# Kernel tuning notes

Measured on AMD Instinct MI355X. Metric: run time of the kernel, lower is better.

Reference implementation:

```python
import jax, jax.numpy as jnp
import numpy as np
from jax import lax

_DN = ('NCHW', 'OIHW', 'NCHW')


def _depthwise_kernel(C):
    base = jnp.array([[0.1, 0.1, 0.1], [0.1, 0.2, 0.1], [0.1, 0.1, 0.1]], jnp.float32)
    return jnp.broadcast_to(base[None, None], (C, 1, 3, 3))


def setup_inputs() -> dict:
    key = jax.random.key(0)
    k0, k1, k2 = jax.random.split(key, 3)
    T, B, C, H, W = 16, 16, 8, 128, 128
    hidden = max(1, C // 16)  # reduction_ratio = 16
    events = jax.random.normal(k0, (T, B, C, H, W), jnp.float32)
    conv_w = _depthwise_kernel(C)  # fixed neighbor kernel from _initialize_weights
    att_w1 = jax.random.normal(k1, (hidden, 2 * C), jnp.float32) / np.sqrt(2 * C)
    att_w2 = jax.random.normal(k2, (C, hidden), jnp.float32) / np.sqrt(hidden)
    return {
        'events': events,
        'conv_w': conv_w,
        'att_w1': att_w1,
        'att_w2': att_w2,
        'density_w': jnp.array(1.0, jnp.float32),
        'temporal_w': jnp.array(0.8, jnp.float32),
        'motion_w': jnp.array(0.5, jnp.float32),
    }


def _forward(events, conv_w, att_w1, att_w2, density_w, temporal_w, motion_w):
    T, B, C, H, W = events.shape
    x = events.reshape(T * B, C, H, W)
    # depthwise 3x3 neighbor conv (groups=C), batched over all T steps at once
    wi = lax.conv_general_dilated(x, conv_w, (1, 1), 'SAME',
                                  dimension_numbers=_DN, feature_group_count=C)
    # --- BALIFBetaAdaptor: max/avg pool -> 1x1 convs (== matmuls) -> sigmoid ---
    mx = jnp.max(x, axis=(2, 3))            # (TB, C)
    av = jnp.mean(x, axis=(2, 3))           # (TB, C)
    pooled = jnp.concatenate([mx, av], axis=1)  # (TB, 2C)
    h = jax.nn.relu(pooled @ att_w1.T)
    beta = (0.5 + 0.45 * jax.nn.sigmoid(h @ att_w2.T)).reshape(T, B, C, 1, 1)
    # --- LightweightEventAdaptor: density / temporal change / unfold variance ---
    density = jnp.mean(x, axis=(1, 2, 3)).reshape(T, B)
    diff = jnp.mean(jnp.abs(events[1:] - events[:-1]), axis=(2, 3, 4))
    temporal = jnp.concatenate([jnp.zeros((1, B), events.dtype), diff], axis=0)  # t=0 -> 0
    # F.unfold(k=3,pad=1) variance over dim=1 (C*9 values, unbiased) via sum-convs
    ones_k = jnp.ones((1, C, 3, 3), events.dtype)
    s1 = lax.conv_general_dilated(x, ones_k, (1, 1), 'SAME', dimension_numbers=_DN)
    s2 = lax.conv_general_dilated(x * x, ones_k, (1, 1), 'SAME', dimension_numbers=_DN)
    n = C * 9
    var = (s2 - s1 * s1 / n) / (n - 1)      # (TB,1,H,W), matches torch.var (ddof=1)
    motion = jnp.mean(var, axis=(1, 2, 3)).reshape(T, B)
    adj = jax.nn.sigmoid(density_w * density + temporal_w * temporal + motion_w * motion) * 2.0
    thr = (1.0 + adj).reshape(T, B, 1, 1, 1)  # base_threshold = 1.0
    wi = wi.reshape(T, B, C, H, W)

    # --- sequential LIF charge/fire/reset (torch.no_grad -> stop_gradient) ---
    def step(v, inp):
        w, b, th, cur = inp
        v = lax.stop_gradient(b * v + (1.0 - b) * w)              # charge
        spike = lax.stop_gradient(jnp.arctan(2.0 * (v - th)) * 0.5 + 0.5)  # atan surrogate
        v = lax.stop_gradient((1.0 - spike) * v)                  # reset (v_reset = 0)
        return v, cur * spike

    v0 = jnp.zeros((B, C, H, W), events.dtype)
    _, out = lax.scan(step, v0, (wi, beta, thr, events))
    return out  # (T,B,C,H,W)


def reference(events, conv_w, att_w1, att_w2, density_w, temporal_w, motion_w):
    return _forward(events, conv_w, att_w1, att_w2, density_w, temporal_w, motion_w)
```

## Files before the change

### kernel.cpp

```cpp
#include <hip/hip_runtime.h>
#include <math.h>

#define T_ 16
#define B_ 16
#define C_ 8
#define H_ 128
#define W_ 128
#define HW_ (H_*W_)
#define CHW_ (C_*HW_)
#define NSLICE 8
#define SR (H_/NSLICE)
#define NV 19

__device__ __forceinline__ float wave_sum(float v){
    #pragma unroll
    for (int o=32;o>0;o>>=1) v += __shfl_down(v,o,64);
    return v;
}
__device__ __forceinline__ float wave_max(float v){
    #pragma unroll
    for (int o=32;o>0;o>>=1) v = fmaxf(v,__shfl_down(v,o,64));
    return v;
}

__global__ __launch_bounds__(256) void stats_kernel(
    const float* __restrict__ events, float* __restrict__ partials)
{
    int raw = blockIdx.x;
    int xcd = raw & 7;
    int q   = raw >> 3;
    int bsel = q >> 7;
    int t    = (q >> 3) & 15;
    int s    = q & 7;
    int b    = xcd + bsel * 8;
    int tb   = t * B_ + b;

    int h0 = s * SR;
    int tid = threadIdx.x;
    const float* frame = events + (size_t)tb * CHW_;
    const float* prev  = frame - (size_t)B_ * CHW_;

    __shared__ float yb[SR+2][W_];
    __shared__ float red[4][NV];

    int cg = tid & 31;
    int c0 = cg * 4;
    int r  = tid >> 5;

    float cnt0 = (c0   == 0 || c0   == W_-1) ? 2.f : 3.f;
    float cnt1 = 3.f;
    float cnt2 = 3.f;
    float cnt3 = (c0+3 == 0 || c0+3 == W_-1) ? 2.f : 3.f;

    float sumc[C_], maxc[C_];
    #pragma unroll
    for (int c=0;c<C_;c++){ sumc[c]=0.f; maxc[c]=-INFINITY; }
    float dsum=0.f, m1=0.f, m2=0.f;

    if (tid < 64){
        int hr = (tid >> 5) ? SR : -1;
        int gh = h0 + hr;
        float y0=0.f,y1=0.f,y2=0.f,y3=0.f;
        if (gh >= 0 && gh < H_){
            const float* rp = frame + gh*W_ + (tid&31)*4;
            #pragma unroll
            for (int c=0;c<C_;c++){
                float4 x = *reinterpret_cast<const float4*>(rp + c*HW_);
                y0+=x.x; y1+=x.y; y2+=x.z; y3+=x.w;
            }
        }
        float* yp = &yb[hr+1][(tid&31)*4];
        yp[0]=y0; yp[1]=y1; yp[2]=y2; yp[3]=y3;
    }

    #pragma unroll 1
    for (int p=0;p<2;p++){
        int lr = r + 8*p;
        int gh = h0 + lr;
        const float* rp = frame + gh*W_ + c0;
        float4 xv[C_];
        #pragma unroll
        for (int c=0;c<C_;c++)
            xv[c] = *reinterpret_cast<const float4*>(rp + c*HW_);

        float y0=0.f,y1=0.f,y2=0.f,y3=0.f;
        float q0=0.f,q1=0.f,q2=0.f,q3=0.f;
        #pragma unroll
        for (int c=0;c<C_;c++){
            float4 x = xv[c];
            y0+=x.x; y1+=x.y; y2+=x.z; y3+=x.w;
            q0=fmaf(x.x,x.x,q0); q1=fmaf(x.y,x.y,q1);
            q2=fmaf(x.z,x.z,q2); q3=fmaf(x.w,x.w,q3);
            sumc[c] += (x.x+x.y)+(x.z+x.w);
            maxc[c] = fmaxf(maxc[c], fmaxf(fmaxf(x.x,x.y),fmaxf(x.z,x.w)));
        }
        float cnth = (gh==0 || gh==H_-1) ? 2.f : 3.f;
        m2 += cnth * (q0*cnt0 + q1*cnt1 + q2*cnt2 + q3*cnt3);

        if (t > 0){
            const float* pp = prev + gh*W_ + c0;
            #pragma unroll
            for (int c=0;c<C_;c++){
                float4 pv = *reinterpret_cast<const float4*>(pp + c*HW_);
                float4 x  = xv[c];
                dsum += fabsf(x.x-pv.x)+fabsf(x.y-pv.y)
                      + fabsf(x.z-pv.z)+fabsf(x.w-pv.w);
            }
        }
        float* yp = &yb[lr+1][c0];
        yp[0]=y0; yp[1]=y1; yp[2]=y2; yp[3]=y3;
    }
    __syncthreads();

    {
        int w  = tid & 127;
        int rg = tid >> 7;
        bool hasL = (w>0), hasR = (w<W_-1);
        int base = rg*8;
        const float* row;
        row = yb[base];   float a0 = row[w] + (hasL?row[w-1]:0.f) + (hasR?row[w+1]:0.f);
        row = yb[base+1]; float a1 = row[w] + (hasL?row[w-1]:0.f) + (hasR?row[w+1]:0.f);
        #pragma unroll
        for (int i=0;i<8;i++){
            row = yb[base+2+i];
            float a2 = row[w] + (hasL?row[w-1]:0.f) + (hasR?row[w+1]:0.f);
            float s1 = a0 + a1 + a2;
            m1 = fmaf(s1, s1, m1);
            a0 = a1; a1 = a2;
        }
    }

    float vals[NV];
    #pragma unroll
    for (int c=0;c<C_;c++){ vals[c]=sumc[c]; vals[8+c]=maxc[c]; }
    vals[16]=dsum; vals[17]=m1; vals[18]=m2;

    int lane = tid & 63, wv = tid >> 6;
    #pragma unroll
    for (int i=0;i<NV;i++){
        float rr = (i>=8 && i<16) ? wave_max(vals[i]) : wave_sum(vals[i]);
        if (lane==0) red[wv][i] = rr;
    }
    __syncthreads();
    if (tid < NV){
        float a = red[0][tid], b2 = red[1][tid], c = red[2][tid], d = red[3][tid];
        float rr = (tid>=8 && tid<16) ? fmaxf(fmaxf(a,b2),fmaxf(c,d)) : ((a+b2)+(c+d));
        partials[((size_t)tb*NSLICE + s)*NV + tid] = rr;
    }
}

__global__ __launch_bounds__(64) void combine_kernel(
    const float* __restrict__ partials,
    const float* __restrict__ att_w1,
    const float* __restrict__ att_w2,
    const float* __restrict__ dwp, const float* __restrict__ twp,
    const float* __restrict__ mwp,
    float* __restrict__ beta_out, float* __restrict__ thr_out,
    float* __restrict__ zeropad)
{
    int tb = blockIdx.x;
    int t  = tb / B_;
    int i  = threadIdx.x;
    if (tb == 0 && i < 16) zeropad[i] = 0.f;
    __shared__ float v[NV];
    if (i < NV){
        const float* p = partials + (size_t)tb*NSLICE*NV;
        bool mx = (i>=8 && i<16);
        float acc = p[i];
        #pragma unroll
        for (int k=1;k<NSLICE;k++){
            float x = p[k*NV + i];
            acc = mx ? fmaxf(acc, x) : (acc + x);
        }
        v[i] = acc;
    }
    __syncthreads();
    if (i == 0){
        float h1 = 0.f;
        for (int c=0;c<C_;c++) h1 += v[8+c] * att_w1[c];
        for (int c=0;c<C_;c++) h1 += (v[c]/(float)HW_) * att_w1[C_+c];
        h1 = fmaxf(h1, 0.f);
        float total = 0.f;
        for (int c=0;c<C_;c++) total += v[c];
        float density  = total / (float)CHW_;
        float temporal = (t==0) ? 0.f : v[16] / (float)CHW_;
        float motion   = (v[18] - v[17]/72.f) / 71.f / (float)HW_;
        float z = dwp[0]*density + twp[0]*temporal + mwp[0]*motion;
        float adj = 2.f / (1.f + expf(-z));
        thr_out[tb] = 1.f + adj;
        for (int c=0;c<C_;c++){
            float sg = 1.f / (1.f + expf(-(h1 * att_w2[c])));
            beta_out[tb*C_ + c] = 0.5f + 0.45f*sg;
        }
    }
}

__device__ __forceinline__ void gload16(const float* src, float* lds_dst){
    __builtin_amdgcn_global_load_lds(
        (const __attribute__((address_space(1))) unsigned int*)src,
        (__attribute__((address_space(3))) unsigned int*)lds_dst, 16, 0, 0);
}

__device__ __forceinline__ float fast_atan(float x){
    float ax = fabsf(x);
    bool inv = ax > 1.f;
    float z  = inv ? __builtin_amdgcn_rcpf(ax) : ax;
    float z2 = z*z;
    float p = -0.0117212f;
    p = fmaf(p, z2,  0.05265332f);
    p = fmaf(p, z2, -0.11643287f);
    p = fmaf(p, z2,  0.19354346f);
    p = fmaf(p, z2, -0.33262347f);
    p = fmaf(p, z2,  0.99997726f);
    p = p * z;
    float r = inv ? (1.57079632679f - p) : p;
    return copysignf(r, x);
}

#define SROWS 10

__global__ __launch_bounds__(256, 8) void lif_kernel(
    const float* __restrict__ events,
    const float* __restrict__ conv_w,
    const float* __restrict__ beta,
    const float* __restrict__ thr,
    const float* __restrict__ zeropad,
    float* __restrict__ out)
{
    int bid  = blockIdx.x;
    int hblk = bid & 15;
    int bc   = bid >> 4;
    int b = bc >> 3, c = bc & 7;
    int h0 = hblk * 8;
    int tid = threadIdx.x;
    int wv  = tid >> 6;

    float wk[9];
    #pragma unroll
    for (int k=0;k<9;k++) wk[k] = conv_w[c*9 + k];

    __shared__ float lds[2][SROWS*W_];

    int idxA = tid,        rowA = idxA >> 5, colA = (idxA & 31) * 4;
    int idxB = 256 + tid,  rowB = idxB >> 5, colB = (idxB & 31) * 4;
    int ghA = h0 - 1 + rowA;
    int ghB = h0 - 1 + rowB;
    bool okA = (ghA >= 0) && (ghA < H_);
    bool okB = (ghB >= 0) && (ghB < H_);
    const float* baseFrame = events + ((size_t)(b * C_) + c) * HW_;
    const float* srcA0 = okA ? (baseFrame + ghA*W_ + colA) : zeropad;
    const float* srcB0 = okB ? (baseFrame + ghB*W_ + colB) : zeropad;
    const size_t tstep = (size_t)B_ * CHW_;
    size_t stepA = okA ? tstep : 0;
    size_t stepB = okB ? tstep : 0;

    int w  = tid & 127;
    int rg = tid >> 7;
    int rbase = rg * 4;
    int wl = (w > 0)    ? w-1 : 0;
    int wr = (w < W_-1) ? w+1 : W_-1;
    bool hasL = (w > 0), hasR = (w < W_-1);

    float v[4];
    #pragma unroll
    for (int i=0;i<4;i++) v[i] = 0.f;

    gload16(srcA0, &lds[0][wv*256]);
    if (wv == 0) gload16(srcB0, &lds[0][1024]);

    const float* bp = beta + (b*C_ + c);
    const float* tp = thr + b;
    float bv = bp[0];
    float th = tp[0];

    for (int t = 0; t < T_; ++t){
        int cur = t & 1, nxt = cur ^ 1;
        __syncthreads();

        if (t + 1 < T_){
            gload16(srcA0 + (size_t)(t+1)*stepA, &lds[nxt][wv*256]);
            if (wv == 0) gload16(srcB0 + (size_t)(t+1)*stepB, &lds[nxt][1024]);
        }
        float bvn = (t+1 < T_) ? bp[(size_t)(t+1)*B_*C_] : 0.f;
        float thn = (t+1 < T_) ? tp[(size_t)(t+1)*B_]    : 0.f;

        const float* L = &lds[cur][0];
        float omb = 1.f - bv;
        float* op = out + ((size_t)(t*B_+b)*C_ + c)*HW_ + h0*W_;

        const float* row0 = L + rbase*W_;
        const float* row1 = row0 + W_;
        float la = hasL ? row0[wl] : 0.f;  float ma = row0[w];  float ra = hasR ? row0[wr] : 0.f;
        float lb = hasL ? row1[wl] : 0.f;  float mb = row1[w];  float rb = hasR ? row1[wr] : 0.f;

        #pragma unroll
        for (int i=0;i<4;i++){
            const float* rowc = L + (rbase+2+i)*W_;
            float lc = hasL ? rowc[wl] : 0.f;
            float mc = rowc[w];
            float rc = hasR ? rowc[wr] : 0.f;
            float wi = wk[0]*la + wk[1]*ma + wk[2]*ra
                     + wk[3]*lb + wk[4]*mb + wk[5]*rb
                     + wk[6]*lc + wk[7]*mc + wk[8]*rc;
            float vv = fmaf(bv, v[i], omb*wi);
            float sp = fast_atan(2.f*(vv - th))*0.5f + 0.5f;
            op[(rbase+i)*W_ + w] = mb * sp;
            v[i] = (1.f - sp) * vv;
            la=lb; ma=mb; ra=rb; lb=lc; mb=mc; rb=rc;
        }
        bv = bvn; th = thn;
    }
}

extern "C" void kernel_launch(void* const* d_in, const int* in_sizes, int n_in,
                              void* d_out, int out_size, void* d_ws, size_t ws_size,
                              hipStream_t stream)
{
    const float* events = (const float*)d_in[0];
    const float* conv_w = (const float*)d_in[1];
    const float* att_w1 = (const float*)d_in[2];
    const float* att_w2 = (const float*)d_in[3];
    const float* dwp    = (const float*)d_in[4];
    const float* twp    = (const float*)d_in[5];
    const float* mwp    = (const float*)d_in[6];
    float* out = (float*)d_out;

    float* ws       = (float*)d_ws;
    float* partials = ws;
    float* beta     = ws + (size_t)T_*B_*NSLICE*NV;
    float* thr      = beta + (size_t)T_*B_*C_;
    float* zeropad  = thr + T_*B_;

    stats_kernel  <<<T_*B_*NSLICE, 256, 0, stream>>>(events, partials);
    combine_kernel<<<T_*B_,        64,  0, stream>>>(partials, att_w1, att_w2,
                                                     dwp, twp, mwp, beta, thr, zeropad);
    lif_kernel    <<<B_*C_*16,     256, 0, stream>>>(events, conv_w, beta, thr, zeropad, out);
}
```

Before: 102.7 us.

## Restructure stats kernel to walk time per block, reusing previous frame in registers

The stats kernel now assigns each block an 8-row slice of one batch image and loops over 8 consecutive time steps. It keeps the previous frame's values in registers for the temporal-difference term instead of reloading them, and prefetches the next step's rows while the current step is being reduced. This removes the second global read of the previous frame and changes the grid to 512 blocks that each run a sequential loop. The trade-offs are two syncthreads per step, higher register pressure from four float4 arrays, and fewer blocks in flight.

```diff
diff --git a/kernel.cpp b/kernel.cpp
--- a/kernel.cpp
+++ b/kernel.cpp
@@ -8,8 +8,9 @@
 #define W_ 128
 #define HW_ (H_*W_)
 #define CHW_ (C_*HW_)
-#define NSLICE 8
-#define SR (H_/NSLICE)
+#define NSL 16
+#define SRW 8
+#define TS 8
 #define NV 19
 
 __device__ __forceinline__ float wave_sum(float v){
@@ -23,129 +24,143 @@
     return v;
 }
 
-__global__ __launch_bounds__(256) void stats_kernel(
+__global__ __launch_bounds__(256, 2) void stats_kernel(
     const float* __restrict__ events, float* __restrict__ partials)
 {
-    int raw = blockIdx.x;
-    int xcd = raw & 7;
-    int q   = raw >> 3;
-    int bsel = q >> 7;
-    int t    = (q >> 3) & 15;
-    int s    = q & 7;
-    int b    = xcd + bsel * 8;
-    int tb   = t * B_ + b;
-
-    int h0 = s * SR;
-    int tid = threadIdx.x;
-    const float* frame = events + (size_t)tb * CHW_;
-    const float* prev  = frame - (size_t)B_ * CHW_;
-
-    __shared__ float yb[SR+2][W_];
+    int bid  = blockIdx.x;
+    int half = bid & 1;
+    int s    = (bid >> 1) & 15;
+    int b    = bid >> 5;
+    int t0   = half * TS;
+    int h0   = s * SRW;
+    int tid  = threadIdx.x;
+
+    int col4 = tid & 31, c0 = col4 * 4;
+    int r    = tid >> 5;
+    int gh   = h0 + r;
+
+    __shared__ float yb[SRW+2][W_];
     __shared__ float red[4][NV];
 
-    int cg = tid & 31;
-    int c0 = cg * 4;
-    int r  = tid >> 5;
-
-    float cnt0 = (c0   == 0 || c0   == W_-1) ? 2.f : 3.f;
-    float cnt1 = 3.f;
-    float cnt2 = 3.f;
-    float cnt3 = (c0+3 == 0 || c0+3 == W_-1) ? 2.f : 3.f;
-
-    float sumc[C_], maxc[C_];
-    #pragma unroll
-    for (int c=0;c<C_;c++){ sumc[c]=0.f; maxc[c]=-INFINITY; }
-    float dsum=0.f, m1=0.f, m2=0.f;
-
-    if (tid < 64){
-        int hr = (tid >> 5) ? SR : -1;
-        int gh = h0 + hr;
-        float y0=0.f,y1=0.f,y2=0.f,y3=0.f;
-        if (gh >= 0 && gh < H_){
-            const float* rp = frame + gh*W_ + (tid&31)*4;
+    int  hsel = tid >> 5;
+    int  hgh  = h0 + (hsel ? SRW : -1);
+    bool hok  = (tid < 64) && (hgh >= 0) && (hgh < H_);
+
+    const size_t fstride = (size_t)B_ * CHW_;
+    const float* own0  = events + (size_t)(t0*B_+b)*CHW_ + gh*W_  + c0;
+    const float* halo0 = events + (size_t)(t0*B_+b)*CHW_ + hgh*W_ + c0;
+
+    float4 cx[C_], px[C_], hx[C_], cx2[C_];
+
+    #pragma unroll
+    for (int c=0;c<C_;c++) cx[c] = *reinterpret_cast<const float4*>(own0 + c*HW_);
+    if (hok){
+        #pragma unroll
+        for (int c=0;c<C_;c++) hx[c] = *reinterpret_cast<const float4*>(halo0 + c*HW_);
+    }
+    if (half){
+        const float* pv = own0 - fstride;
+        #pragma unroll
+        for (int c=0;c<C_;c++) px[c] = *reinterpret_cast<const float4*>(pv + c*HW_);
+    } else {
+        #pragma unroll
+        for (int c=0;c<C_;c++){ px[c].x=0.f; px[c].y=0.f; px[c].z=0.f; px[c].w=0.f; }
+    }
+
+    float cnt0 = (c0==0)     ? 2.f : 3.f;
+    float cnt3 = (c0+3==W_-1)? 2.f : 3.f;
+    float cnth = (gh==0 || gh==H_-1) ? 2.f : 3.f;
+
+    #pragma unroll 1
+    for (int tt=0; tt<TS; ++tt){
+        int t = t0 + tt;
+
+        float sumc[C_], maxc[C_];
+        float4 y; y.x=0.f; y.y=0.f; y.z=0.f; y.w=0.f;
+        float q0=0.f,q1=0.f,q2=0.f,q3=0.f;
+        float dsum = 0.f;
+        #pragma unroll
+        for (int c=0;c<C_;c++){
+            float4 x = cx[c];
+            y.x+=x.x; y.y+=x.y; y.z+=x.z; y.w+=x.w;
+            q0=fmaf(x.x,x.x,q0); q1=fmaf(x.y,x.y,q1);
+            q2=fmaf(x.z,x.z,q2); q3=fmaf(x.w,x.w,q3);
+            sumc[c] = (x.x+x.y)+(x.z+x.w);
+            maxc[c] = fmaxf(fmaxf(x.x,x.y),fmaxf(x.z,x.w));
+        }
+        float m2 = cnth * (q0*cnt0 + (q1+q2)*3.f + q3*cnt3);
+        if (t > 0){
             #pragma unroll
             for (int c=0;c<C_;c++){
-                float4 x = *reinterpret_cast<const float4*>(rp + c*HW_);
-                y0+=x.x; y1+=x.y; y2+=x.z; y3+=x.w;
+                float4 x = cx[c], p = px[c];
+                dsum += fabsf(x.x-p.x)+fabsf(x.y-p.y)
+                      + fabsf(x.z-p.z)+fabsf(x.w-p.w);
             }
         }
-        float* yp = &yb[hr+1][(tid&31)*4];
-        yp[0]=y0; yp[1]=y1; yp[2]=y2; yp[3]=y3;
-    }
-
-    #pragma unroll 1
-    for (int p=0;p<2;p++){
-        int lr = r + 8*p;
-        int gh = h0 + lr;
-        const float* rp = frame + gh*W_ + c0;
-        float4 xv[C_];
-        #pragma unroll
-        for (int c=0;c<C_;c++)
-            xv[c] = *reinterpret_cast<const float4*>(rp + c*HW_);
-
-        float y0=0.f,y1=0.f,y2=0.f,y3=0.f;
-        float q0=0.f,q1=0.f,q2=0.f,q3=0.f;
-        #pragma unroll
-        for (int c=0;c<C_;c++){
-            float4 x = xv[c];
-            y0+=x.x; y1+=x.y; y2+=x.z; y3+=x.w;
-            q0=fmaf(x.x,x.x,q0); q1=fmaf(x.y,x.y,q1);
-            q2=fmaf(x.z,x.z,q2); q3=fmaf(x.w,x.w,q3);
-            sumc[c] += (x.x+x.y)+(x.z+x.w);
-            maxc[c] = fmaxf(maxc[c], fmaxf(fmaxf(x.x,x.y),fmaxf(x.z,x.w)));
-        }
-        float cnth = (gh==0 || gh==H_-1) ? 2.f : 3.f;
-        m2 += cnth * (q0*cnt0 + q1*cnt1 + q2*cnt2 + q3*cnt3);
-
-        if (t > 0){
-            const float* pp = prev + gh*W_ + c0;
+        #pragma unroll
+        for (int c=0;c<C_;c++) px[c] = cx[c];
+
+        *reinterpret_cast<float4*>(&yb[r+1][c0]) = y;
+        if (tid < 64){
+            float4 hy; hy.x=0.f; hy.y=0.f; hy.z=0.f; hy.w=0.f;
+            if (hok){
+                #pragma unroll
+                for (int c=0;c<C_;c++){
+                    float4 x = hx[c];
+                    hy.x+=x.x; hy.y+=x.y; hy.z+=x.z; hy.w+=x.w;
+                }
+            }
+            *reinterpret_cast<float4*>(&yb[hsel ? SRW+1 : 0][c0]) = hy;
+        }
+        __syncthreads();
+
+        {
+            int tn = (tt+1 < TS) ? (tt+1) : tt;
+            const float* op = own0 + (size_t)tn*fstride;
             #pragma unroll
-            for (int c=0;c<C_;c++){
-                float4 pv = *reinterpret_cast<const float4*>(pp + c*HW_);
-                float4 x  = xv[c];
-                dsum += fabsf(x.x-pv.x)+fabsf(x.y-pv.y)
-                      + fabsf(x.z-pv.z)+fabsf(x.w-pv.w);
+            for (int c=0;c<C_;c++) cx2[c] = *reinterpret_cast<const float4*>(op + c*HW_);
+            if (hok){
+                const float* hp = halo0 + (size_t)tn*fstride;
+                #pragma unroll
+                for (int c=0;c<C_;c++) hx[c] = *reinterpret_cast<const float4*>(hp + c*HW_);
             }
         }
-        float* yp = &yb[lr+1][c0];
-        yp[0]=y0; yp[1]=y1; yp[2]=y2; yp[3]=y3;
-    }
-    __syncthreads();
-
-    {
-        int w  = tid & 127;
-        int rg = tid >> 7;
-        bool hasL = (w>0), hasR = (w<W_-1);
-        int base = rg*8;
-        const float* row;
-        row = yb[base];   float a0 = row[w] + (hasL?row[w-1]:0.f) + (hasR?row[w+1]:0.f);
-        row = yb[base+1]; float a1 = row[w] + (hasL?row[w-1]:0.f) + (hasR?row[w+1]:0.f);
-        #pragma unroll
-        for (int i=0;i<8;i++){
-            row = yb[base+2+i];
-            float a2 = row[w] + (hasL?row[w-1]:0.f) + (hasR?row[w+1]:0.f);
-            float s1 = a0 + a1 + a2;
-            m1 = fmaf(s1, s1, m1);
-            a0 = a1; a1 = a2;
-        }
-    }
-
-    float vals[NV];
-    #pragma unroll
-    for (int c=0;c<C_;c++){ vals[c]=sumc[c]; vals[8+c]=maxc[c]; }
-    vals[16]=dsum; vals[17]=m1; vals[18]=m2;
-
-    int lane = tid & 63, wv = tid >> 6;
-    #pragma unroll
-    for (int i=0;i<NV;i++){
-        float rr = (i>=8 && i<16) ? wave_max(vals[i]) : wave_sum(vals[i]);
-        if (lane==0) red[wv][i] = rr;
-    }
-    __syncthreads();
-    if (tid < NV){
-        float a = red[0][tid], b2 = red[1][tid], c = red[2][tid], d = red[3][tid];
-        float rr = (tid>=8 && tid<16) ? fmaxf(fmaxf(a,b2),fmaxf(c,d)) : ((a+b2)+(c+d));
-        partials[((size_t)tb*NSLICE + s)*NV + tid] = rr;
+
+        float m1;
+        {
+            float4 v0 = *reinterpret_cast<const float4*>(&yb[r  ][c0]);
+            float4 v1 = *reinterpret_cast<const float4*>(&yb[r+1][c0]);
+            float4 v2 = *reinterpret_cast<const float4*>(&yb[r+2][c0]);
+            float4 vv; vv.x=v0.x+v1.x+v2.x; vv.y=v0.y+v1.y+v2.y;
+                       vv.z=v0.z+v1.z+v2.z; vv.w=v0.w+v1.w+v2.w;
+            float vL = (c0>0)      ? yb[r][c0-1]+yb[r+1][c0-1]+yb[r+2][c0-1] : 0.f;
+            float vR = (c0+4<W_)   ? yb[r][c0+4]+yb[r+1][c0+4]+yb[r+2][c0+4] : 0.f;
+            float s1x = vL  +vv.x+vv.y;
+            float s1y = vv.x+vv.y+vv.z;
+            float s1z = vv.y+vv.z+vv.w;
+            float s1w = vv.z+vv.w+vR;
+            m1 = s1x*s1x + s1y*s1y + s1z*s1z + s1w*s1w;
+        }
+
+        float vals[NV];
+        #pragma unroll
+        for (int c=0;c<C_;c++){ vals[c]=sumc[c]; vals[8+c]=maxc[c]; }
+        vals[16]=dsum; vals[17]=m1; vals[18]=m2;
+
+        int lane = tid & 63, wv = tid >> 6;
+        #pragma unroll
+        for (int i=0;i<NV;i++){
+            float rr = (i>=8 && i<16) ? wave_max(vals[i]) : wave_sum(vals[i]);
+            if (lane==0) red[wv][i] = rr;
+        }
+        __syncthreads();
+        if (tid < NV){
+            float a = red[0][tid], b2 = red[1][tid], c = red[2][tid], d = red[3][tid];
+            float rr = (tid>=8 && tid<16) ? fmaxf(fmaxf(a,b2),fmaxf(c,d)) : ((a+b2)+(c+d));
+            partials[((size_t)(t*B_+b)*NSL + s)*NV + tid] = rr;
+        }
+        #pragma unroll
+        for (int c=0;c<C_;c++) cx[c] = cx2[c];
     }
 }
 
@@ -164,11 +179,11 @@
     if (tb == 0 && i < 16) zeropad[i] = 0.f;
     __shared__ float v[NV];
     if (i < NV){
-        const float* p = partials + (size_t)tb*NSLICE*NV;
+        const float* p = partials + (size_t)tb*NSL*NV;
         bool mx = (i>=8 && i<16);
         float acc = p[i];
         #pragma unroll
-        for (int k=1;k<NSLICE;k++){
+        for (int k=1;k<NSL;k++){
             float x = p[k*NV + i];
             acc = mx ? fmaxf(acc, x) : (acc + x);
         }
@@ -327,12 +342,12 @@
 
     float* ws       = (float*)d_ws;
     float* partials = ws;
-    float* beta     = ws + (size_t)T_*B_*NSLICE*NV;
+    float* beta     = ws + (size_t)T_*B_*NSL*NV;
     float* thr      = beta + (size_t)T_*B_*C_;
     float* zeropad  = thr + T_*B_;
 
-    stats_kernel  <<<T_*B_*NSLICE, 256, 0, stream>>>(events, partials);
-    combine_kernel<<<T_*B_,        64,  0, stream>>>(partials, att_w1, att_w2,
-                                                     dwp, twp, mwp, beta, thr, zeropad);
-    lif_kernel    <<<B_*C_*16,     256, 0, stream>>>(events, conv_w, beta, thr, zeropad, out);
-}
+    stats_kernel  <<<B_*NSL*2,  256, 0, stream>>>(events, partials);
+    combine_kernel<<<T_*B_,     64,  0, stream>>>(partials, att_w1, att_w2,
+                                                  dwp, twp, mwp, beta, thr, zeropad);
+    lif_kernel    <<<B_*C_*16,  256, 0, stream>>>(events, conv_w, beta, thr, zeropad, out);
+}
```

Result: slower. 106.2 us (+3.4%).

## Split stats into halo-free streaming pass plus separate channel-sum stencil kernel

Applied to the files above, without the earlier changes.

The stats kernel no longer loads halo rows and does no shared-memory stencil. Each thread handles one row-chunk, writes the channel-summed field to a workspace buffer, and reduces the per-frame statistics over 16 slices. A new m1 kernel reads that field back with halos to compute the squared 3x3 box-sum term, and combine now merges both sets of partials. The intent is to drop the redundant halo reads and raise occupancy in the bandwidth-heavy pass, at the cost of an extra launch, a 16MB field write and read, and an added __syncthreads inside the LIF time loop.

```diff
diff --git a/kernel.cpp b/kernel.cpp
--- a/kernel.cpp
+++ b/kernel.cpp
@@ -8,8 +8,7 @@
 #define W_ 128
 #define HW_ (H_*W_)
 #define CHW_ (C_*HW_)
-#define NSLICE 8
-#define SR (H_/NSLICE)
+#define NSL 16
 #define NV 19
 
 __device__ __forceinline__ float wave_sum(float v){
@@ -23,95 +22,97 @@
     return v;
 }
 
-__global__ __launch_bounds__(256) void stats_kernel(
-    const float* __restrict__ events, float* __restrict__ partials)
-{
-    int raw = blockIdx.x;
-    int xcd = raw & 7;
-    int q   = raw >> 3;
-    int bsel = q >> 7;
-    int t    = (q >> 3) & 15;
-    int s    = q & 7;
-    int b    = xcd + bsel * 8;
-    int tb   = t * B_ + b;
-
-    int h0 = s * SR;
+__global__ __launch_bounds__(256, 4) void stats_stream_kernel(
+    const float* __restrict__ events, float* __restrict__ partials,
+    float* __restrict__ yfield)
+{
+    int bid = blockIdx.x;
+    int s   = bid & 15;
+    int tb  = bid >> 4;
+    int t   = tb >> 4;
     int tid = threadIdx.x;
-    const float* frame = events + (size_t)tb * CHW_;
-    const float* prev  = frame - (size_t)B_ * CHW_;
-
-    __shared__ float yb[SR+2][W_];
-    __shared__ float red[4][NV];
-
-    int cg = tid & 31;
-    int c0 = cg * 4;
-    int r  = tid >> 5;
-
-    float cnt0 = (c0   == 0 || c0   == W_-1) ? 2.f : 3.f;
-    float cnt1 = 3.f;
-    float cnt2 = 3.f;
-    float cnt3 = (c0+3 == 0 || c0+3 == W_-1) ? 2.f : 3.f;
-
-    float sumc[C_], maxc[C_];
-    #pragma unroll
-    for (int c=0;c<C_;c++){ sumc[c]=0.f; maxc[c]=-INFINITY; }
-    float dsum=0.f, m1=0.f, m2=0.f;
-
-    if (tid < 64){
-        int hr = (tid >> 5) ? SR : -1;
-        int gh = h0 + hr;
-        float y0=0.f,y1=0.f,y2=0.f,y3=0.f;
-        if (gh >= 0 && gh < H_){
-            const float* rp = frame + gh*W_ + (tid&31)*4;
-            #pragma unroll
-            for (int c=0;c<C_;c++){
-                float4 x = *reinterpret_cast<const float4*>(rp + c*HW_);
-                y0+=x.x; y1+=x.y; y2+=x.z; y3+=x.w;
-            }
-        }
-        float* yp = &yb[hr+1][(tid&31)*4];
-        yp[0]=y0; yp[1]=y1; yp[2]=y2; yp[3]=y3;
-    }
-
-    #pragma unroll 1
-    for (int p=0;p<2;p++){
-        int lr = r + 8*p;
-        int gh = h0 + lr;
-        const float* rp = frame + gh*W_ + c0;
-        float4 xv[C_];
-        #pragma unroll
-        for (int c=0;c<C_;c++)
-            xv[c] = *reinterpret_cast<const float4*>(rp + c*HW_);
-
-        float y0=0.f,y1=0.f,y2=0.f,y3=0.f;
-        float q0=0.f,q1=0.f,q2=0.f,q3=0.f;
+    int r   = tid >> 5;
+    int c0  = (tid & 31) * 4;
+    int gh  = s*8 + r;
+
+    const float* frame = events + (size_t)tb*CHW_ + gh*W_ + c0;
+    const float* prev  = frame - (size_t)B_*CHW_;
+
+    float4 xv[C_];
+    #pragma unroll
+    for (int c=0;c<C_;c++) xv[c] = *reinterpret_cast<const float4*>(frame + c*HW_);
+
+    float dsum = 0.f;
+    if (t > 0){
         #pragma unroll
         for (int c=0;c<C_;c++){
+            float4 p = *reinterpret_cast<const float4*>(prev + c*HW_);
             float4 x = xv[c];
-            y0+=x.x; y1+=x.y; y2+=x.z; y3+=x.w;
-            q0=fmaf(x.x,x.x,q0); q1=fmaf(x.y,x.y,q1);
-            q2=fmaf(x.z,x.z,q2); q3=fmaf(x.w,x.w,q3);
-            sumc[c] += (x.x+x.y)+(x.z+x.w);
-            maxc[c] = fmaxf(maxc[c], fmaxf(fmaxf(x.x,x.y),fmaxf(x.z,x.w)));
-        }
-        float cnth = (gh==0 || gh==H_-1) ? 2.f : 3.f;
-        m2 += cnth * (q0*cnt0 + q1*cnt1 + q2*cnt2 + q3*cnt3);
-
-        if (t > 0){
-            const float* pp = prev + gh*W_ + c0;
-            #pragma unroll
-            for (int c=0;c<C_;c++){
-                float4 pv = *reinterpret_cast<const float4*>(pp + c*HW_);
-                float4 x  = xv[c];
-                dsum += fabsf(x.x-pv.x)+fabsf(x.y-pv.y)
-                      + fabsf(x.z-pv.z)+fabsf(x.w-pv.w);
-            }
-        }
-        float* yp = &yb[lr+1][c0];
-        yp[0]=y0; yp[1]=y1; yp[2]=y2; yp[3]=y3;
+            dsum += fabsf(x.x-p.x)+fabsf(x.y-p.y)
+                  + fabsf(x.z-p.z)+fabsf(x.w-p.w);
+        }
+    }
+
+    float sumc[C_], maxc[C_];
+    float4 y; y.x=0.f; y.y=0.f; y.z=0.f; y.w=0.f;
+    float q0=0.f,q1=0.f,q2=0.f,q3=0.f;
+    #pragma unroll
+    for (int c=0;c<C_;c++){
+        float4 x = xv[c];
+        y.x+=x.x; y.y+=x.y; y.z+=x.z; y.w+=x.w;
+        q0=fmaf(x.x,x.x,q0); q1=fmaf(x.y,x.y,q1);
+        q2=fmaf(x.z,x.z,q2); q3=fmaf(x.w,x.w,q3);
+        sumc[c] = (x.x+x.y)+(x.z+x.w);
+        maxc[c] = fmaxf(fmaxf(x.x,x.y),fmaxf(x.z,x.w));
+    }
+    float cnt0 = (c0==0)      ? 2.f : 3.f;
+    float cnt3 = (c0+3==W_-1) ? 2.f : 3.f;
+    float cnth = (gh==0 || gh==H_-1) ? 2.f : 3.f;
+    float m2 = cnth * (q0*cnt0 + (q1+q2)*3.f + q3*cnt3);
+
+    *reinterpret_cast<float4*>(yfield + (size_t)tb*HW_ + gh*W_ + c0) = y;
+
+    float vals[NV];
+    #pragma unroll
+    for (int c=0;c<C_;c++){ vals[c]=sumc[c]; vals[8+c]=maxc[c]; }
+    vals[16]=dsum; vals[17]=0.f; vals[18]=m2;
+
+    __shared__ float red[4][NV];
+    int lane = tid & 63, wv = tid >> 6;
+    #pragma unroll
+    for (int i=0;i<NV;i++){
+        float rr = (i>=8 && i<16) ? wave_max(vals[i]) : wave_sum(vals[i]);
+        if (lane==0) red[wv][i] = rr;
     }
     __syncthreads();
-
+    if (tid < NV){
+        float a = red[0][tid], b2 = red[1][tid], c = red[2][tid], d = red[3][tid];
+        float rr = (tid>=8 && tid<16) ? fmaxf(fmaxf(a,b2),fmaxf(c,d)) : ((a+b2)+(c+d));
+        partials[((size_t)tb*NSL + s)*NV + tid] = rr;
+    }
+}
+
+__global__ __launch_bounds__(256) void m1_kernel(
+    const float* __restrict__ yfield, float* __restrict__ m1p)
+{
+    int bid = blockIdx.x;
+    int s   = bid & 7;
+    int tb  = bid >> 3;
+    int h0  = s*16;
+    int tid = threadIdx.x;
+    __shared__ float yb[18][W_];
+
+    const float* yf = yfield + (size_t)tb*HW_;
+    for (int i = tid; i < 18*32; i += 256){
+        int rr = i >> 5, cc = (i & 31) * 4;
+        int gh = h0 - 1 + rr;
+        float4 v; v.x=0.f; v.y=0.f; v.z=0.f; v.w=0.f;
+        if (gh >= 0 && gh < H_) v = *reinterpret_cast<const float4*>(yf + gh*W_ + cc);
+        *reinterpret_cast<float4*>(&yb[rr][cc]) = v;
+    }
+    __syncthreads();
+
+    float m1 = 0.f;
     {
         int w  = tid & 127;
         int rg = tid >> 7;
@@ -129,28 +130,17 @@
             a0 = a1; a1 = a2;
         }
     }
-
-    float vals[NV];
-    #pragma unroll
-    for (int c=0;c<C_;c++){ vals[c]=sumc[c]; vals[8+c]=maxc[c]; }
-    vals[16]=dsum; vals[17]=m1; vals[18]=m2;
-
+    m1 = wave_sum(m1);
+    __shared__ float red2[4];
     int lane = tid & 63, wv = tid >> 6;
-    #pragma unroll
-    for (int i=0;i<NV;i++){
-        float rr = (i>=8 && i<16) ? wave_max(vals[i]) : wave_sum(vals[i]);
-        if (lane==0) red[wv][i] = rr;
-    }
+    if (lane==0) red2[wv] = m1;
     __syncthreads();
-    if (tid < NV){
-        float a = red[0][tid], b2 = red[1][tid], c = red[2][tid], d = red[3][tid];
-        float rr = (tid>=8 && tid<16) ? fmaxf(fmaxf(a,b2),fmaxf(c,d)) : ((a+b2)+(c+d));
-        partials[((size_t)tb*NSLICE + s)*NV + tid] = rr;
-    }
+    if (tid==0) m1p[bid] = (red2[0]+red2[1])+(red2[2]+red2[3]);
 }
 
 __global__ __launch_bounds__(64) void combine_kernel(
     const float* __restrict__ partials,
+    const float* __restrict__ m1p,
     const float* __restrict__ att_w1,
     const float* __restrict__ att_w2,
     const float* __restrict__ dwp, const float* __restrict__ twp,
@@ -164,15 +154,23 @@
     if (tb == 0 && i < 16) zeropad[i] = 0.f;
     __shared__ float v[NV];
     if (i < NV){
-        const float* p = partials + (size_t)tb*NSLICE*NV;
-        bool mx = (i>=8 && i<16);
-        float acc = p[i];
-        #pragma unroll
-        for (int k=1;k<NSLICE;k++){
-            float x = p[k*NV + i];
-            acc = mx ? fmaxf(acc, x) : (acc + x);
-        }
-        v[i] = acc;
+        if (i == 17){
+            const float* mp = m1p + (size_t)tb*8;
+            float acc = 0.f;
+            #pragma unroll
+            for (int k=0;k<8;k++) acc += mp[k];
+            v[17] = acc;
+        } else {
+            const float* p = partials + (size_t)tb*NSL*NV;
+            bool mx = (i>=8 && i<16);
+            float acc = p[i];
+            #pragma unroll
+            for (int k=1;k<NSL;k++){
+                float x = p[k*NV + i];
+                acc = mx ? fmaxf(acc, x) : (acc + x);
+            }
+            v[i] = acc;
+        }
     }
     __syncthreads();
     if (i == 0){
@@ -308,6 +306,8 @@
             v[i] = (1.f - sp) * vv;
             la=lb; ma=mb; ra=rb; lb=lc; mb=mc; rb=rc;
         }
+        __syncthreads();
+
         bv = bvn; th = thn;
     }
 }
@@ -327,12 +327,15 @@
 
     float* ws       = (float*)d_ws;
     float* partials = ws;
-    float* beta     = ws + (size_t)T_*B_*NSLICE*NV;
+    float* m1p      = partials + (size_t)T_*B_*NSL*NV;
+    float* beta     = m1p + (size_t)T_*B_*8;
     float* thr      = beta + (size_t)T_*B_*C_;
     float* zeropad  = thr + T_*B_;
-
-    stats_kernel  <<<T_*B_*NSLICE, 256, 0, stream>>>(events, partials);
-    combine_kernel<<<T_*B_,        64,  0, stream>>>(partials, att_w1, att_w2,
-                                                     dwp, twp, mwp, beta, thr, zeropad);
-    lif_kernel    <<<B_*C_*16,     256, 0, stream>>>(events, conv_w, beta, thr, zeropad, out);
-}
+    float* yfield   = zeropad + 16;
+
+    stats_stream_kernel<<<T_*B_*NSL, 256, 0, stream>>>(events, partials, yfield);
+    m1_kernel          <<<T_*B_*8,   256, 0, stream>>>(yfield, m1p);
+    combine_kernel     <<<T_*B_,     64,  0, stream>>>(partials, m1p, att_w1, att_w2,
+                                                       dwp, twp, mwp, beta, thr, zeropad);
+    lif_kernel         <<<B_*C_*16,  256, 0, stream>>>(events, conv_w, beta, thr, zeropad, out);
+}
```

After: 100.3 us. 1.02x faster.
